# Optimization experiments

Hardware: AMD Instinct MI355X
Metric: run time of the kernel (lower is better)

The kernel has to match this reference:

```python
import jax, jax.numpy as jnp
import numpy as np

BN_EPS = 1e-5
N_OUT, D_OUT = 64, 128


def setup_inputs() -> dict:
    key = jax.random.key(0)
    k1, k2, k3, k4 = jax.random.split(key, 4)
    B, N_in, D_in, K = 512, 64, 128, 4
    x = jax.random.normal(k1, (B, N_in, D_in), dtype=jnp.float32)
    # block-sparse weights: one (D_in x D_out) block per (output-row, active-input-row) pair
    W = jax.random.normal(k2, (N_OUT, K, D_in, D_OUT), dtype=jnp.float32) * (1.0 / np.sqrt(K * D_in))
    bias = jax.random.normal(k3, (N_OUT, D_OUT), dtype=jnp.float32) * 0.02
    gamma = jnp.ones((N_OUT * D_OUT,), dtype=jnp.float32)
    beta = jnp.zeros((N_OUT * D_OUT,), dtype=jnp.float32)
    idx = jax.random.randint(k4, (N_OUT, K), 0, N_in, dtype=jnp.int32)
    return {"x": x, "W": W, "bias": bias, "gamma": gamma, "beta": beta, "idx": idx}


def reference(x, W, bias, gamma, beta, idx):
    B = x.shape[0]
    # structured-sparse linear: gather active input rows, per-block matmul
    xg = x[:, idx, :]                                   # [B, N_out, K, D_in]
    y = jnp.einsum('bokd,okde->boe', xg, W) + bias      # [B, N_out, D_out]
    # BatchNorm1d (training-mode batch statistics) on flattened features
    yf = y.reshape(B, -1)                               # [B, N_out*D_out]
    mean = jnp.mean(yf, axis=0)
    var = jnp.mean(jnp.square(yf - mean), axis=0)       # biased variance, as in torch BN
    yn = (yf - mean) * jax.lax.rsqrt(var + BN_EPS) * gamma + beta
    # Swish: z * sigmoid(z)
    out = yn * jax.nn.sigmoid(yn)
    return out.reshape(B, N_OUT, D_OUT)
```

## Files before the change

kernel.cpp:

```cpp
#include <hip/hip_runtime.h>


typedef __attribute__((ext_vector_type(8))) __bf16 bf16x8;
typedef __attribute__((ext_vector_type(4))) __bf16 bf16x4;
typedef __attribute__((ext_vector_type(4))) float  f32x4;

#define B_SZ   512
#define N_IN   64
#define D_IN   128
#define N_O    64
#define D_O    128
#define FEAT   (N_O * D_O)
#define LDA    40

__global__ __launch_bounds__(256, 2)
void gemm_stats_kernel(const float* __restrict__ x, const float* __restrict__ W,
                       const float* __restrict__ bias, const int* __restrict__ idxp,
                       __bf16* __restrict__ y, float* __restrict__ psum,
                       float* __restrict__ psq)
{
    __shared__ __bf16 Alds[64 * LDA];
    __shared__ __bf16 Blds[128 * LDA];

    const int bx   = blockIdx.x;
    const int o    = bx >> 3;
    const int bt   = bx & 7;
    const int b0   = bt * 64;
    const int tid  = threadIdx.x;
    const int wave = tid >> 6;
    const int lane = tid & 63;
    const int lam  = lane & 15;
    const int quad = lane >> 4;

    int rsel[4];
#pragma unroll
    for (int k = 0; k < 4; ++k) rsel[k] = idxp[o * 4 + k];

    const f32x4 zero4 = {0.f, 0.f, 0.f, 0.f};
    f32x4 acc[4][2];
#pragma unroll
    for (int mi = 0; mi < 4; ++mi)
#pragma unroll
        for (int ni = 0; ni < 2; ++ni) acc[mi][ni] = zero4;

    const int m_a = tid >> 2;
    const int ca  = (tid & 3) * 8;

    for (int kk = 0; kk < 16; ++kk) {
        const int kidx = kk >> 2;
        const int d0   = (kk & 3) * 32;
        const int r    = rsel[kidx];

        const float* xa = x + (((b0 + m_a) * N_IN + r) * D_IN + d0 + ca);
        f32x4 xv0 = *(const f32x4*)(xa + 0);
        f32x4 xv1 = *(const f32x4*)(xa + 4);
        bf16x8 p0;
        p0[0] = (__bf16)xv0[0]; p0[1] = (__bf16)xv0[1];
        p0[2] = (__bf16)xv0[2]; p0[3] = (__bf16)xv0[3];
        p0[4] = (__bf16)xv1[0]; p0[5] = (__bf16)xv1[1];
        p0[6] = (__bf16)xv1[2]; p0[7] = (__bf16)xv1[3];

        bf16x4 wb[4];
        int te[4], tdg[4];
#pragma unroll
        for (int it = 0; it < 4; ++it) {
            const int task = it * 256 + tid;
            const int e  = task & 127;
            const int dg = task >> 7;
            te[it] = e; tdg[it] = dg;
            const float* wp = W + (((o * 4 + kidx) * 128 + (d0 + dg * 4)) * 128 + e);
            wb[it][0] = (__bf16)wp[0];
            wb[it][1] = (__bf16)wp[128];
            wb[it][2] = (__bf16)wp[256];
            wb[it][3] = (__bf16)wp[384];
        }

        __syncthreads();
        *(bf16x8*)&Alds[m_a * LDA + ca] = p0;
#pragma unroll
        for (int it = 0; it < 4; ++it)
            *(bf16x4*)&Blds[te[it] * LDA + tdg[it] * 4] = wb[it];
        __syncthreads();

        bf16x8 af[4], bfv[2];
#pragma unroll
        for (int mi = 0; mi < 4; ++mi)
            af[mi] = *(const bf16x8*)&Alds[(mi * 16 + lam) * LDA + quad * 8];
#pragma unroll
        for (int ni = 0; ni < 2; ++ni)
            bfv[ni] = *(const bf16x8*)&Blds[(wave * 32 + ni * 16 + lam) * LDA + quad * 8];
#pragma unroll
        for (int mi = 0; mi < 4; ++mi)
#pragma unroll
            for (int ni = 0; ni < 2; ++ni)
                acc[mi][ni] = __builtin_amdgcn_mfma_f32_16x16x32_bf16(
                    af[mi], bfv[ni], acc[mi][ni], 0, 0, 0);
    }

    const int nbase = wave * 32;
    float bvals[2];
#pragma unroll
    for (int ni = 0; ni < 2; ++ni)
        bvals[ni] = bias[o * 128 + nbase + ni * 16 + lam];

#pragma unroll
    for (int mi = 0; mi < 4; ++mi)
#pragma unroll
        for (int ni = 0; ni < 2; ++ni)
#pragma unroll
            for (int rr = 0; rr < 4; ++rr) acc[mi][ni][rr] += bvals[ni];

#pragma unroll
    for (int mi = 0; mi < 4; ++mi) {
        const int mrow = b0 + mi * 16 + quad * 4;
#pragma unroll
        for (int ni = 0; ni < 2; ++ni) {
            const int col = o * 128 + nbase + ni * 16 + lam;
#pragma unroll
            for (int rr = 0; rr < 4; ++rr)
                y[(mrow + rr) * FEAT + col] = (__bf16)acc[mi][ni][rr];
        }
    }

#pragma unroll
    for (int ni = 0; ni < 2; ++ni) {
        float s = 0.f, q = 0.f;
#pragma unroll
        for (int mi = 0; mi < 4; ++mi)
#pragma unroll
            for (int rr = 0; rr < 4; ++rr) {
                const float v = acc[mi][ni][rr];
                s += v; q += v * v;
            }
        s += __shfl_xor(s, 16); s += __shfl_xor(s, 32);
        q += __shfl_xor(q, 16); q += __shfl_xor(q, 32);
        if (quad == 0) {
            const int e = nbase + ni * 16 + lam;
            psum[(o * 8 + bt) * 128 + e] = s;
            psq [(o * 8 + bt) * 128 + e] = q;
        }
    }
}

__global__ __launch_bounds__(256, 4)
void norm_silu_kernel(const __bf16* __restrict__ y, const float* __restrict__ psum,
                      const float* __restrict__ psq, const float* __restrict__ gamma,
                      const float* __restrict__ beta, float* __restrict__ out)
{
    __shared__ float sscale[128];
    __shared__ float sshift[128];
    const int o   = blockIdx.x >> 3;
    const int bc  = blockIdx.x & 7;
    const int tid = threadIdx.x;

    if (tid < 128) {
        float s = 0.f, q = 0.f;
#pragma unroll
        for (int sl = 0; sl < 8; ++sl) {
            s += psum[(o * 8 + sl) * 128 + tid];
            q += psq [(o * 8 + sl) * 128 + tid];
        }
        const float mean = s * (1.0f / 512.0f);
        const float var  = q * (1.0f / 512.0f) - mean * mean;
        const float rstd = rsqrtf(var + 1e-5f);
        const float sc   = rstd * gamma[o * 128 + tid];
        sscale[tid] = sc;
        sshift[tid] = beta[o * 128 + tid] - mean * sc;
    }
    __syncthreads();

#pragma unroll
    for (int it = 0; it < 4; ++it) {
        const int lin = it * 2048 + tid * 8;
        const int bl  = lin >> 7;
        const int e   = lin & 127;
        const int g   = (bc * 64 + bl) * FEAT + o * 128 + e;
        bf16x8 y8 = *(const bf16x8*)&y[g];
        f32x4 ov0, ov1;
#pragma unroll
        for (int j = 0; j < 4; ++j) {
            const float v  = (float)y8[j];
            const float xn = v * sscale[e + j] + sshift[e + j];
            ov0[j] = xn / (1.0f + __expf(-xn));
        }
#pragma unroll
        for (int j = 0; j < 4; ++j) {
            const float v  = (float)y8[4 + j];
            const float xn = v * sscale[e + 4 + j] + sshift[e + 4 + j];
            ov1[j] = xn / (1.0f + __expf(-xn));
        }
        *(f32x4*)&out[g]     = ov0;
        *(f32x4*)&out[g + 4] = ov1;
    }
}

extern "C" void kernel_launch(void* const* d_in, const int* in_sizes, int n_in,
                              void* d_out, int out_size, void* d_ws, size_t ws_size,
                              hipStream_t stream)
{
    const float* x     = (const float*)d_in[0];
    const float* W     = (const float*)d_in[1];
    const float* bias  = (const float*)d_in[2];
    const float* gamma = (const float*)d_in[3];
    const float* beta  = (const float*)d_in[4];
    const int*   idx   = (const int*)d_in[5];
    float* out = (float*)d_out;

    __bf16* y   = (__bf16*)d_ws;
    float* psum = (float*)((char*)d_ws + (size_t)B_SZ * FEAT * sizeof(__bf16));
    float* psq  = psum + 64 * 8 * 128;

    gemm_stats_kernel<<<dim3(512), dim3(256), 0, stream>>>(x, W, bias, idx, y, psum, psq);
    norm_silu_kernel<<<dim3(512), dim3(256), 0, stream>>>(y, psum, psq, gamma, beta, out);
}
```

Baseline: 112.4 us.

## Pre-transpose weights to bf16 MFMA layout and double-buffer A tile

```diff
diff --git a/kernel.cpp b/kernel.cpp
--- a/kernel.cpp
+++ b/kernel.cpp
@@ -8,19 +8,52 @@
 #define B_SZ   512
 #define N_IN   64
 #define D_IN   128
-#define N_O    64
-#define D_O    128
-#define FEAT   (N_O * D_O)
+#define FEAT   8192
 #define LDA    40
+#define LDT    130
 
 __global__ __launch_bounds__(256, 2)
-void gemm_stats_kernel(const float* __restrict__ x, const float* __restrict__ W,
+void prep_w_kernel(const float* __restrict__ W, __bf16* __restrict__ Wt2)
+{
+    __shared__ __bf16 T[128 * LDT];
+    const int o    = blockIdx.x >> 2;
+    const int kidx = blockIdx.x & 3;
+    const int tid  = threadIdx.x;
+
+#pragma unroll
+    for (int it = 0; it < 16; ++it) {
+        const int lin = it * 1024 + tid * 4;
+        const int d   = lin >> 7;
+        const int e   = lin & 127;
+        f32x4 v = *(const f32x4*)(W + (((o * 4 + kidx) * 128 + d) * 128 + e));
+        bf16x4 b;
+        b[0] = (__bf16)v[0]; b[1] = (__bf16)v[1];
+        b[2] = (__bf16)v[2]; b[3] = (__bf16)v[3];
+        *(bf16x4*)&T[d * LDT + e] = b;
+    }
+    __syncthreads();
+
+#pragma unroll
+    for (int it = 0; it < 8; ++it) {
+        const int task = it * 256 + tid;
+        const int e    = task >> 4;
+        const int dc   = task & 15;
+        bf16x8 v;
+#pragma unroll
+        for (int j = 0; j < 8; ++j) v[j] = T[(dc * 8 + j) * LDT + e];
+        const int kk  = kidx * 4 + (dc >> 2);
+        const int kin = (dc & 3) * 8;
+        *(bf16x8*)(Wt2 + (((o * 16 + kk) * 128 + e) * 32 + kin)) = v;
+    }
+}
+
+__global__ __launch_bounds__(256, 2)
+void gemm_stats_kernel(const float* __restrict__ x, const __bf16* __restrict__ Wt2,
                        const float* __restrict__ bias, const int* __restrict__ idxp,
                        __bf16* __restrict__ y, float* __restrict__ psum,
                        float* __restrict__ psq)
 {
-    __shared__ __bf16 Alds[64 * LDA];
-    __shared__ __bf16 Blds[128 * LDA];
+    __shared__ __bf16 Alds[2][64 * LDA];
 
     const int bx   = blockIdx.x;
     const int o    = bx >> 3;
@@ -31,6 +64,7 @@
     const int lane = tid & 63;
     const int lam  = lane & 15;
     const int quad = lane >> 4;
+    const int nbase = wave * 32;
 
     int rsel[4];
 #pragma unroll
@@ -46,49 +80,45 @@
     const int m_a = tid >> 2;
     const int ca  = (tid & 3) * 8;
 
+    const __bf16* bptr = Wt2 + ((size_t)(o * 16) * 128 + nbase + lam) * 32 + quad * 8;
+
+    f32x4 xv0, xv1;
+    {
+        const int r = rsel[0];
+        const float* xa = x + (((b0 + m_a) * N_IN + r) * D_IN + ca);
+        xv0 = *(const f32x4*)(xa + 0);
+        xv1 = *(const f32x4*)(xa + 4);
+    }
+
     for (int kk = 0; kk < 16; ++kk) {
-        const int kidx = kk >> 2;
-        const int d0   = (kk & 3) * 32;
-        const int r    = rsel[kidx];
-
-        const float* xa = x + (((b0 + m_a) * N_IN + r) * D_IN + d0 + ca);
-        f32x4 xv0 = *(const f32x4*)(xa + 0);
-        f32x4 xv1 = *(const f32x4*)(xa + 4);
-        bf16x8 p0;
-        p0[0] = (__bf16)xv0[0]; p0[1] = (__bf16)xv0[1];
-        p0[2] = (__bf16)xv0[2]; p0[3] = (__bf16)xv0[3];
-        p0[4] = (__bf16)xv1[0]; p0[5] = (__bf16)xv1[1];
-        p0[6] = (__bf16)xv1[2]; p0[7] = (__bf16)xv1[3];
-
-        bf16x4 wb[4];
-        int te[4], tdg[4];
-#pragma unroll
-        for (int it = 0; it < 4; ++it) {
-            const int task = it * 256 + tid;
-            const int e  = task & 127;
-            const int dg = task >> 7;
-            te[it] = e; tdg[it] = dg;
-            const float* wp = W + (((o * 4 + kidx) * 128 + (d0 + dg * 4)) * 128 + e);
-            wb[it][0] = (__bf16)wp[0];
-            wb[it][1] = (__bf16)wp[128];
-            wb[it][2] = (__bf16)wp[256];
-            wb[it][3] = (__bf16)wp[384];
-        }
-
+        bf16x8 p;
+        p[0] = (__bf16)xv0[0]; p[1] = (__bf16)xv0[1];
+        p[2] = (__bf16)xv0[2]; p[3] = (__bf16)xv0[3];
+        p[4] = (__bf16)xv1[0]; p[5] = (__bf16)xv1[1];
+        p[6] = (__bf16)xv1[2]; p[7] = (__bf16)xv1[3];
+        const int buf = kk & 1;
+        *(bf16x8*)&Alds[buf][m_a * LDA + ca] = p;
         __syncthreads();
-        *(bf16x8*)&Alds[m_a * LDA + ca] = p0;
-#pragma unroll
-        for (int it = 0; it < 4; ++it)
-            *(bf16x4*)&Blds[te[it] * LDA + tdg[it] * 4] = wb[it];
-        __syncthreads();
-
-        bf16x8 af[4], bfv[2];
+
+        if (kk < 15) {
+            const int kn = kk + 1;
+            const int r  = rsel[kn >> 2];
+            const int d0 = (kn & 3) * 32;
+            const float* xa = x + (((b0 + m_a) * N_IN + r) * D_IN + d0 + ca);
+            xv0 = *(const f32x4*)(xa + 0);
+            xv1 = *(const f32x4*)(xa + 4);
+        }
+
+        bf16x8 bfv[2];
+#pragma unroll
+        for (int ni = 0; ni < 2; ++ni)
+            bfv[ni] = *(const bf16x8*)(bptr + ((size_t)kk * 128 + ni * 16) * 32);
+
+        bf16x8 af[4];
 #pragma unroll
         for (int mi = 0; mi < 4; ++mi)
-            af[mi] = *(const bf16x8*)&Alds[(mi * 16 + lam) * LDA + quad * 8];
-#pragma unroll
-        for (int ni = 0; ni < 2; ++ni)
-            bfv[ni] = *(const bf16x8*)&Blds[(wave * 32 + ni * 16 + lam) * LDA + quad * 8];
+            af[mi] = *(const bf16x8*)&Alds[buf][(mi * 16 + lam) * LDA + quad * 8];
+
 #pragma unroll
         for (int mi = 0; mi < 4; ++mi)
 #pragma unroll
@@ -97,7 +127,6 @@
                     af[mi], bfv[ni], acc[mi][ni], 0, 0, 0);
     }
 
-    const int nbase = wave * 32;
     float bvals[2];
 #pragma unroll
     for (int ni = 0; ni < 2; ++ni)
@@ -206,10 +235,12 @@
     const int*   idx   = (const int*)d_in[5];
     float* out = (float*)d_out;
 
-    __bf16* y   = (__bf16*)d_ws;
-    float* psum = (float*)((char*)d_ws + (size_t)B_SZ * FEAT * sizeof(__bf16));
-    float* psq  = psum + 64 * 8 * 128;
-
-    gemm_stats_kernel<<<dim3(512), dim3(256), 0, stream>>>(x, W, bias, idx, y, psum, psq);
+    __bf16* y    = (__bf16*)d_ws;
+    __bf16* Wt2  = y + (size_t)B_SZ * FEAT;
+    float*  psum = (float*)(Wt2 + (size_t)64 * 512 * 128);
+    float*  psq  = psum + 64 * 8 * 128;
+
+    prep_w_kernel<<<dim3(256), dim3(256), 0, stream>>>(W, Wt2);
+    gemm_stats_kernel<<<dim3(512), dim3(256), 0, stream>>>(x, Wt2, bias, idx, y, psum, psq);
     norm_silu_kernel<<<dim3(512), dim3(256), 0, stream>>>(y, psum, psq, gamma, beta, out);
 }
```

After: 109.5 us. 1.03x faster.
